# Kernel tuning notes

Hardware: AMD Instinct MI355X
Metric: run time of the kernel (lower is better)

## Reference

```python
import jax, jax.numpy as jnp
import numpy as np

FEAT = 64
K = 16
K4 = K // 4
EPS = 1e-5  # BatchNorm eps (inference mode with running stats)


def _conv1x1(x, w, b):
    # x: (B, Cin, N, K), w: (Cout, Cin), b: (Cout,)
    return jnp.einsum('oc,bcnk->bonk', w, x) + b[None, :, None, None]


def _bn(x, g, be, m, v):
    # inference-mode BatchNorm2d over channel axis 1
    inv = g / jnp.sqrt(v + EPS)
    return (x - m[None, :, None, None]) * inv[None, :, None, None] + be[None, :, None, None]


def setup_inputs() -> dict:
    key = jax.random.key(0)
    ks = jax.random.split(key, 20)
    B, N, M = 4, 8192, 8192
    d = {}
    d['original_pts'] = jax.random.normal(ks[0], (B, 3, M), dtype=jnp.float32)
    d['query_pts'] = jax.random.normal(ks[1], (B, 3, N), dtype=jnp.float32)
    d['local_feat'] = jax.random.normal(ks[2], (B, FEAT, M), dtype=jnp.float32)
    # mlp_0: Conv2D(3, FEAT) with BN + ReLU
    d['w0'] = jax.random.normal(ks[3], (FEAT, 3), dtype=jnp.float32) * 0.2
    d['b0'] = jax.random.normal(ks[4], (FEAT,), dtype=jnp.float32) * 0.01
    d['g0'] = 1.0 + 0.1 * jax.random.normal(ks[5], (FEAT,), dtype=jnp.float32)
    d['be0'] = 0.01 * jax.random.normal(ks[6], (FEAT,), dtype=jnp.float32)
    d['m0'] = 0.01 * jax.random.normal(ks[7], (FEAT,), dtype=jnp.float32)
    d['v0'] = jax.random.uniform(ks[8], (FEAT,), dtype=jnp.float32, minval=0.5, maxval=1.5)
    # mlp_1: Conv2D(FEAT, FEAT) with BN + ReLU
    d['w1'] = jax.random.normal(ks[9], (FEAT, FEAT), dtype=jnp.float32) * 0.1
    d['b1'] = jax.random.normal(ks[10], (FEAT,), dtype=jnp.float32) * 0.01
    d['g1'] = 1.0 + 0.1 * jax.random.normal(ks[11], (FEAT,), dtype=jnp.float32)
    d['be1'] = 0.01 * jax.random.normal(ks[12], (FEAT,), dtype=jnp.float32)
    d['m1'] = 0.01 * jax.random.normal(ks[13], (FEAT,), dtype=jnp.float32)
    d['v1'] = jax.random.uniform(ks[14], (FEAT,), dtype=jnp.float32, minval=0.5, maxval=1.5)
    # mlp_2: Conv2D(2*FEAT, 1), no BN, no ReLU
    d['w2'] = jax.random.normal(ks[15], (1, 2 * FEAT), dtype=jnp.float32) * 0.1
    d['b2'] = jax.random.normal(ks[16], (1,), dtype=jnp.float32) * 0.01
    return d


def reference(original_pts, query_pts, local_feat,
              w0, b0, g0, be0, m0, v0,
              w1, b1, g1, be1, m1, v1,
              w2, b2):
    B, _, N = query_pts.shape
    # --- KNN: squared distances (B, N, M), take K smallest ---
    q2 = jnp.sum(query_pts ** 2, axis=1)          # (B, N)
    o2 = jnp.sum(original_pts ** 2, axis=1)       # (B, M)
    cross = jnp.einsum('bcn,bcm->bnm', query_pts, original_pts)
    d2 = q2[:, :, None] + o2[:, None, :] - 2.0 * cross
    _, knn_idx = jax.lax.top_k(-d2, K)            # (B, N, K)

    # gather neighbor coords: (B, 3, N, K)
    knn_pts = jax.vmap(lambda pts, idx: pts[:, idx])(original_pts, knn_idx)
    # gather local features for first K//4 neighbors: (B, FEAT, N, K4)
    patch_feat = jax.vmap(lambda f, idx: f[:, idx])(local_feat, knn_idx[:, :, :K4])

    relative_pts = knn_pts - query_pts[:, :, :, None]  # (B, 3, N, K)
    feat0 = jax.nn.relu(_bn(_conv1x1(relative_pts, w0, b0), g0, be0, m0, v0))  # (B, F, N, K)
    feat_g = jnp.max(feat0, axis=3, keepdims=True)                              # (B, F, N, 1)
    relative_feat = jax.nn.relu(_bn(_conv1x1(feat0, w1, b1), g1, be1, m1, v1))[:, :, :, :K4]
    feat2 = jnp.concatenate(
        [relative_feat, jnp.broadcast_to(feat_g, (B, FEAT, N, K4))], axis=1)    # (B, 2F, N, K4)
    weight = jax.nn.sigmoid(_conv1x1(feat2, w2, b2))                            # (B, 1, N, K4)
    query_feat = (1.0 - weight) * relative_feat + weight * patch_feat
    return jnp.sum(query_feat, axis=-1)  # (B, FEAT, N)
```

## Files before the change

### kernel.cpp

```cpp
#include <hip/hip_runtime.h>
#include <cstdint>

#define M_PTS 8192
#define N_QRY 8192
#define BATCH 4

typedef unsigned long long ull;

__device__ __forceinline__ float d2_exact(float qx, float qy, float qz, float q2, float4 p) {
#pragma clang fp contract(off)
  float dot = (qx * p.x + qy * p.y) + qz * p.z;
  return (q2 + p.w) - 2.0f * dot;
}

__device__ __forceinline__ unsigned flipf(float d) {
  unsigned u = __float_as_uint(d);
  return u ^ ((unsigned)((int)u >> 31) | 0x80000000u);
}

__device__ __forceinline__ int lane_prefix(unsigned long long m) {
  return __builtin_amdgcn_mbcnt_hi((unsigned)(m >> 32),
         __builtin_amdgcn_mbcnt_lo((unsigned)m, 0));
}

__device__ __forceinline__ void ld_lds16(const float4* g, float4* l) {
  __builtin_amdgcn_global_load_lds((const __attribute__((address_space(1))) void*)g,
                                   (__attribute__((address_space(3))) void*)l, 16, 0, 0);
}

__device__ __forceinline__ float tau16(float mn) {
  float lo = mn, hi = mn;
#pragma unroll
  for (int j = 1; j < 64; j <<= 1) {
    lo = fminf(lo, __shfl_xor(lo, j));
    hi = fmaxf(hi, __shfl_xor(hi, j));
  }
#pragma unroll
  for (int it = 0; it < 10; it++) {
    float mid = 0.5f * (lo + hi);
    int cnt = __popcll(__ballot(mn <= mid));
    if (cnt >= 16) hi = mid; else lo = mid;
  }
  return hi;
}

__device__ __forceinline__ ull bsort64(ull v, int lane) {
#pragma unroll
  for (int k = 2; k <= 64; k <<= 1) {
#pragma unroll
    for (int j = k >> 1; j >= 1; j >>= 1) {
      ull o = __shfl_xor(v, j);
      bool keepmin = (((lane & k) == 0) == ((lane & j) == 0));
      ull lo = v < o ? v : o;
      ull hi = v < o ? o : v;
      v = keepmin ? lo : hi;
    }
  }
  return v;
}

__global__ void prep_kernel(const float* __restrict__ original_pts,
                            const float* __restrict__ query_pts,
                            const float* __restrict__ lf,
                            float4* __restrict__ pp, float4* __restrict__ qp,
                            float* __restrict__ lfT) {
#pragma clang fp contract(off)
  const int bid = blockIdx.x;
  if (bid < 256) {
    const float* src = (bid < 128) ? original_pts : query_pts;
    float4* dst = (bid < 128) ? pp : qp;
    int i = (bid & 127) * 256 + threadIdx.x;
    int b = i >> 13, m = i & (M_PTS - 1);
    const float* s = src + (size_t)b * 3 * M_PTS;
    float x = s[m], y = s[M_PTS + m], z = s[2 * M_PTS + m];
    float ss = (x * x + y * y) + z * z;
    dst[i] = make_float4(x, y, z, ss);
    return;
  }
  __shared__ float tile[64][65];
  int vbid = bid - 256;
  int bb = vbid >> 7;
  int m0 = (vbid & 127) << 6;
  int tm = threadIdx.x & 63;
  int tc = threadIdx.x >> 6;
  const float* src = lf + (size_t)bb * 64 * M_PTS;
#pragma unroll
  for (int i = 0; i < 16; i++) {
    int ch = i * 4 + tc;
    tile[ch][tm] = src[(size_t)ch * M_PTS + m0 + tm];
  }
  __syncthreads();
  float* dst = lfT + ((size_t)bb * M_PTS + m0) * 64;
#pragma unroll
  for (int i = 0; i < 16; i++) {
    int mm = i * 4 + tc;
    dst[(size_t)mm * 64 + tm] = tile[tm][mm];
  }
}

__global__ void __launch_bounds__(512, 8) knn_kernel(const float4* __restrict__ pp,
                                                     const float4* __restrict__ qp,
                                                     int* __restrict__ knn_out,
                                                     int qbase) {
  __shared__ float4 spts[2][512];
  __shared__ ull cbuf[16][96];
  const int tid = threadIdx.x;
  const int lane = tid & 63;
  const int wave = tid >> 6;
  const int qa = qbase + blockIdx.x * 16 + wave * 2;
  const int b = qa >> 13;
  const float4* pb = pp + ((size_t)b << 13);

  const float4 A4 = qp[qa];
  const float4 B4 = qp[qa + 1];
  const float axA = -2.0f * A4.x, ayA = -2.0f * A4.y, azA = -2.0f * A4.z;
  const float axB = -2.0f * B4.x, ayB = -2.0f * B4.y, azB = -2.0f * B4.z;

  int cntA = 0, cntB = 0;
  unsigned* cqA = (unsigned*)cbuf[wave * 2 + 0];
  unsigned* cqB = (unsigned*)cbuf[wave * 2 + 1];

  float mnA = 3.402823466e38f, mnB = 3.402823466e38f;
  float tauA = 0.0f, tauB = 0.0f;

  auto stage = [&](float4* dst, int s) {
    const float4* g = pb + s * 512 + wave * 64 + lane;
    ld_lds16(g, &dst[wave * 64]);
  };

  auto minpass = [&](const float4* sp) {
#pragma unroll
    for (int j = 0; j < 8; j++) {
      float4 p = sp[j * 64 + lane];
      mnA = fminf(mnA, __builtin_fmaf(axA, p.x, __builtin_fmaf(ayA, p.y,
                       __builtin_fmaf(azA, p.z, p.w))));
      mnB = fminf(mnB, __builtin_fmaf(axB, p.x, __builtin_fmaf(ayB, p.y,
                       __builtin_fmaf(azB, p.z, p.w))));
    }
  };

  auto collect = [&](float e, float tau, unsigned* cq, int& cnt, unsigned idx) {
    bool pred = e <= tau;
    unsigned long long mask = __ballot(pred);
    if (mask) {
      int pos = cnt + lane_prefix(mask);
      if (pred && pos < 192) cq[pos] = idx;
      cnt += __popcll(mask);
    }
  };

  auto fused = [&](const float4* sp, unsigned base) {
#pragma unroll
    for (int j = 0; j < 8; j++) {
      float4 p = sp[j * 64 + lane];
      float ea = __builtin_fmaf(axA, p.x, __builtin_fmaf(ayA, p.y,
                 __builtin_fmaf(azA, p.z, p.w)));
      float eb = __builtin_fmaf(axB, p.x, __builtin_fmaf(ayB, p.y,
                 __builtin_fmaf(azB, p.z, p.w)));
      mnA = fminf(mnA, ea);
      mnB = fminf(mnB, eb);
      unsigned idx = base + j * 64 + lane;
      collect(ea, tauA, cqA, cntA, idx);
      collect(eb, tauB, cqB, cntB, idx);
    }
  };

  stage(spts[0], 0);
  __syncthreads();
  stage(spts[1], 1);
  minpass(spts[0]);
  __syncthreads();
  minpass(spts[1]);
  tauA = tau16(mnA) + 0.01f;
  tauB = tau16(mnB) + 0.01f;
  fused(spts[0], 0);
  fused(spts[1], 512);
  __syncthreads();
  stage(spts[0], 2);
  __syncthreads();

  for (int s = 2; s < 16; ++s) {
    if (s < 15) stage(spts[(s + 1) & 1], s + 1);
    fused(spts[s & 1], (unsigned)(s * 512));
    if (s == 3 || s == 7 || s == 11) {
      tauA = fminf(tauA, tau16(mnA) + 0.01f);
      tauB = fminf(tauB, tau16(mnB) + 0.01f);
    }
    __syncthreads();
  }

  auto finalize = [&](ull* cb, int cnt, int gq,
                      float qx, float qy, float qz, float q2) {
    unsigned* cu = (unsigned*)cb;
    int E = cnt < 192 ? cnt : 192;
    unsigned i0 = (lane < E) ? cu[lane] : 0u;
    unsigned i1 = (lane + 64 < E) ? cu[lane + 64] : 0u;
    unsigned i2 = (lane + 128 < E) ? cu[lane + 128] : 0u;
    float4 p0 = pb[i0];
    float4 p1 = pb[i1];
    float4 p2 = pb[i2];
    ull k0 = ~0ull, k1 = ~0ull, k2 = ~0ull;
    if (lane < E)
      k0 = ((ull)flipf(d2_exact(qx, qy, qz, q2, p0)) << 32) | i0;
    if (lane + 64 < E)
      k1 = ((ull)flipf(d2_exact(qx, qy, qz, q2, p1)) << 32) | i1;
    if (lane + 128 < E)
      k2 = ((ull)flipf(d2_exact(qx, qy, qz, q2, p2)) << 32) | i2;
    ull ml = k0 < k1 ? k0 : k1;
    if (k2 < ml) ml = k2;
    ull T = __shfl(bsort64(ml, lane), 15);
    int c2 = 0;
    {
      bool pr = k0 <= T; ull m = __ballot(pr);
      int pos = c2 + lane_prefix(m);
      if (pr) cb[pos] = k0;
      c2 += __popcll(m);
    }
    {
      bool pr = k1 <= T; ull m = __ballot(pr);
      int pos = c2 + lane_prefix(m);
      if (pr) cb[pos] = k1;
      c2 += __popcll(m);
    }
    {
      bool pr = k2 <= T; ull m = __ballot(pr);
      int pos = c2 + lane_prefix(m);
      if (pr) cb[pos] = k2;
      c2 += __popcll(m);
    }
    ull kk = (lane < c2) ? cb[lane] : ~0ull;
    ull fin = bsort64(kk, lane);
    if (lane < 16) knn_out[(size_t)gq * 16 + lane] = (int)(unsigned)fin;
  };

  finalize(cbuf[wave * 2 + 0], cntA, qa,     A4.x, A4.y, A4.z, A4.w);
  finalize(cbuf[wave * 2 + 1], cntB, qa + 1, B4.x, B4.y, B4.z, B4.w);
}

__global__ void __launch_bounds__(512) feat_kernel(
    const float4* __restrict__ pp, const float4* __restrict__ qp,
    const int* __restrict__ knn, const float* __restrict__ lfT,
    const float* __restrict__ w0, const float* __restrict__ b0,
    const float* __restrict__ g0, const float* __restrict__ be0,
    const float* __restrict__ m0, const float* __restrict__ v0,
    const float* __restrict__ w1, const float* __restrict__ b1,
    const float* __restrict__ g1, const float* __restrict__ be1,
    const float* __restrict__ m1, const float* __restrict__ v1,
    const float* __restrict__ w2, const float* __restrict__ b2,
    float* __restrict__ out) {
  __shared__ float w1T[64][65];
  __shared__ float4 relbuf[8][16];
  __shared__ float4 f0v[8][64];
  __shared__ float outbuf[64][33];
  const int tid = threadIdx.x;
  const int lane = tid & 63;
  const int wave = tid >> 6;
  const int gq0 = blockIdx.x * 32;
  const int b = gq0 >> 13;

  {
    const float4* w1f4 = (const float4*)w1;
#pragma unroll
    for (int k = 0; k < 2; k++) {
      int linear4 = tid + k * 512;
      int c = linear4 >> 4;
      int c2 = (linear4 & 15) * 4;
      float4 t = w1f4[linear4];
      w1T[c2 + 0][c] = t.x;
      w1T[c2 + 1][c] = t.y;
      w1T[c2 + 2][c] = t.z;
      w1T[c2 + 3][c] = t.w;
    }
  }

  const float inv0 = g0[lane] / sqrtf(v0[lane] + 1e-5f);
  const float w00 = w0[lane * 3 + 0] * inv0;
  const float w01 = w0[lane * 3 + 1] * inv0;
  const float w02 = w0[lane * 3 + 2] * inv0;
  const float bb0 = (b0[lane] - m0[lane]) * inv0 + be0[lane];
  const float inv1 = g1[lane] / sqrtf(v1[lane] + 1e-5f);
  const float bb1 = (b1[lane] - m1[lane]) * inv1 + be1[lane];

  const float w2a = w2[lane], w2b = w2[64 + lane];
  const float bias2 = b2[0];
  const float4* pb = pp + ((size_t)b << 13);
  const float* lfb = lfT + (((size_t)b << 13)) * 64;

  __syncthreads();

  for (int qi = 0; qi < 4; qi++) {
    const int gq = gq0 + wave * 4 + qi;
    const float4 q4 = qp[gq];
    int nk = knn[(size_t)gq * 16 + (lane & 15)];
    float4 pk = pb[nk];
    int i0 = __shfl(nk, 0), i1 = __shfl(nk, 1), i2 = __shfl(nk, 2), i3 = __shfl(nk, 3);
    float p0 = lfb[(size_t)i0 * 64 + lane];
    float p1 = lfb[(size_t)i1 * 64 + lane];
    float p2 = lfb[(size_t)i2 * 64 + lane];
    float p3 = lfb[(size_t)i3 * 64 + lane];

    if (lane < 16)
      relbuf[wave][lane] = make_float4(pk.x - q4.x, pk.y - q4.y, pk.z - q4.z, 0.0f);

    float g = 0.0f, f0 = 0, f1 = 0, f2 = 0, f3 = 0;
#pragma unroll
    for (int k = 0; k < 16; k++) {
      float4 r = relbuf[wave][k];
      float y = fmaxf(0.0f, w00 * r.x + w01 * r.y + w02 * r.z + bb0);
      g = fmaxf(g, y);
      if (k == 0) f0 = y; else if (k == 1) f1 = y;
      else if (k == 2) f2 = y; else if (k == 3) f3 = y;
    }
    f0v[wave][lane] = make_float4(f0, f1, f2, f3);

    float a0 = 0, a1 = 0, a2 = 0, a3 = 0;
#pragma unroll
    for (int c2 = 0; c2 < 64; c2++) {
      float w = w1T[c2][lane];
      float4 fb = f0v[wave][c2];
      a0 = fmaf(w, fb.x, a0); a1 = fmaf(w, fb.y, a1);
      a2 = fmaf(w, fb.z, a2); a3 = fmaf(w, fb.w, a3);
    }
    float r0 = fmaxf(0.0f, fmaf(a0, inv1, bb1));
    float r1 = fmaxf(0.0f, fmaf(a1, inv1, bb1));
    float r2 = fmaxf(0.0f, fmaf(a2, inv1, bb1));
    float r3 = fmaxf(0.0f, fmaf(a3, inv1, bb1));

    float s0 = w2a * r0, s1 = w2a * r1, s2 = w2a * r2, s3 = w2a * r3, tg = w2b * g;
#pragma unroll
    for (int j = 1; j < 64; j <<= 1) {
      s0 += __shfl_xor(s0, j);
      s1 += __shfl_xor(s1, j);
      s2 += __shfl_xor(s2, j);
      s3 += __shfl_xor(s3, j);
      tg += __shfl_xor(tg, j);
    }
    float wk0 = 1.0f / (1.0f + __expf(-(s0 + tg + bias2)));
    float wk1 = 1.0f / (1.0f + __expf(-(s1 + tg + bias2)));
    float wk2 = 1.0f / (1.0f + __expf(-(s2 + tg + bias2)));
    float wk3 = 1.0f / (1.0f + __expf(-(s3 + tg + bias2)));

    float oc = ((1.0f - wk0) * r0 + wk0 * p0)
             + ((1.0f - wk1) * r1 + wk1 * p1)
             + ((1.0f - wk2) * r2 + wk2 * p2)
             + ((1.0f - wk3) * r3 + wk3 * p3);
    outbuf[lane][wave * 4 + qi] = oc;
  }
  __syncthreads();

  int c = tid >> 3, j = tid & 7;
  float4 o4 = make_float4(outbuf[c][j * 4 + 0], outbuf[c][j * 4 + 1],
                          outbuf[c][j * 4 + 2], outbuf[c][j * 4 + 3]);
  *(float4*)(out + (((size_t)(b * 64 + c)) << 13) + (gq0 & (N_QRY - 1)) + j * 4) = o4;
}

extern "C" void kernel_launch(void* const* d_in, const int* in_sizes, int n_in,
                              void* d_out, int out_size, void* d_ws, size_t ws_size,
                              hipStream_t stream) {
  (void)in_sizes; (void)n_in; (void)out_size; (void)ws_size;
  const float* original_pts = (const float*)d_in[0];
  const float* query_pts   = (const float*)d_in[1];
  const float* local_feat  = (const float*)d_in[2];
  const float* w0 = (const float*)d_in[3];
  const float* b0 = (const float*)d_in[4];
  const float* g0 = (const float*)d_in[5];
  const float* be0 = (const float*)d_in[6];
  const float* m0 = (const float*)d_in[7];
  const float* v0 = (const float*)d_in[8];
  const float* w1 = (const float*)d_in[9];
  const float* b1 = (const float*)d_in[10];
  const float* g1 = (const float*)d_in[11];
  const float* be1 = (const float*)d_in[12];
  const float* m1 = (const float*)d_in[13];
  const float* v1 = (const float*)d_in[14];
  const float* w2 = (const float*)d_in[15];
  const float* b2 = (const float*)d_in[16];
  float* out = (float*)d_out;

  char* ws = (char*)d_ws;
  float4* pp  = (float4*)(ws);
  float4* qp  = (float4*)(ws + 524288);
  float*  lfT = (float*)(ws + 1048576);
  int*    knn = (int*)(ws + 9437184);

  prep_kernel<<<768, 256, 0, stream>>>(original_pts, query_pts, local_feat,
                                       pp, qp, lfT);
  knn_kernel<<<1024, 512, 0, stream>>>(pp, qp, knn, 0);
  knn_kernel<<<1024, 512, 0, stream>>>(pp, qp, knn, 16384);
  feat_kernel<<<1024, 512, 0, stream>>>(pp, qp, knn, lfT,
                                        w0, b0, g0, be0, m0, v0,
                                        w1, b1, g1, be1, m1, v1,
                                        w2, b2, out);
}
```

Before: 255.2 us.

## Fuse KNN search and feature MLP into one kernel with shared-memory neighbor indices

Merges the two KNN launches and the feature kernel into a single kernel. Each block finds neighbors for 16 queries, keeps the indices in shared memory, then reuses an aliased shared buffer for the MLP stage. This removes the global KNN index round trip and two launch boundaries. In exchange the union shared-memory footprint (about 31 KB) may lower occupancy for the KNN phase, the w1 transpose setup is now repeated in twice as many blocks, and the output store uses only half the threads.

```diff
diff --git a/kernel.cpp b/kernel.cpp
--- a/kernel.cpp
+++ b/kernel.cpp
@@ -98,148 +98,9 @@
   }
 }
 
-__global__ void __launch_bounds__(512, 8) knn_kernel(const float4* __restrict__ pp,
-                                                     const float4* __restrict__ qp,
-                                                     int* __restrict__ knn_out,
-                                                     int qbase) {
-  __shared__ float4 spts[2][512];
-  __shared__ ull cbuf[16][96];
-  const int tid = threadIdx.x;
-  const int lane = tid & 63;
-  const int wave = tid >> 6;
-  const int qa = qbase + blockIdx.x * 16 + wave * 2;
-  const int b = qa >> 13;
-  const float4* pb = pp + ((size_t)b << 13);
-
-  const float4 A4 = qp[qa];
-  const float4 B4 = qp[qa + 1];
-  const float axA = -2.0f * A4.x, ayA = -2.0f * A4.y, azA = -2.0f * A4.z;
-  const float axB = -2.0f * B4.x, ayB = -2.0f * B4.y, azB = -2.0f * B4.z;
-
-  int cntA = 0, cntB = 0;
-  unsigned* cqA = (unsigned*)cbuf[wave * 2 + 0];
-  unsigned* cqB = (unsigned*)cbuf[wave * 2 + 1];
-
-  float mnA = 3.402823466e38f, mnB = 3.402823466e38f;
-  float tauA = 0.0f, tauB = 0.0f;
-
-  auto stage = [&](float4* dst, int s) {
-    const float4* g = pb + s * 512 + wave * 64 + lane;
-    ld_lds16(g, &dst[wave * 64]);
-  };
-
-  auto minpass = [&](const float4* sp) {
-#pragma unroll
-    for (int j = 0; j < 8; j++) {
-      float4 p = sp[j * 64 + lane];
-      mnA = fminf(mnA, __builtin_fmaf(axA, p.x, __builtin_fmaf(ayA, p.y,
-                       __builtin_fmaf(azA, p.z, p.w))));
-      mnB = fminf(mnB, __builtin_fmaf(axB, p.x, __builtin_fmaf(ayB, p.y,
-                       __builtin_fmaf(azB, p.z, p.w))));
-    }
-  };
-
-  auto collect = [&](float e, float tau, unsigned* cq, int& cnt, unsigned idx) {
-    bool pred = e <= tau;
-    unsigned long long mask = __ballot(pred);
-    if (mask) {
-      int pos = cnt + lane_prefix(mask);
-      if (pred && pos < 192) cq[pos] = idx;
-      cnt += __popcll(mask);
-    }
-  };
-
-  auto fused = [&](const float4* sp, unsigned base) {
-#pragma unroll
-    for (int j = 0; j < 8; j++) {
-      float4 p = sp[j * 64 + lane];
-      float ea = __builtin_fmaf(axA, p.x, __builtin_fmaf(ayA, p.y,
-                 __builtin_fmaf(azA, p.z, p.w)));
-      float eb = __builtin_fmaf(axB, p.x, __builtin_fmaf(ayB, p.y,
-                 __builtin_fmaf(azB, p.z, p.w)));
-      mnA = fminf(mnA, ea);
-      mnB = fminf(mnB, eb);
-      unsigned idx = base + j * 64 + lane;
-      collect(ea, tauA, cqA, cntA, idx);
-      collect(eb, tauB, cqB, cntB, idx);
-    }
-  };
-
-  stage(spts[0], 0);
-  __syncthreads();
-  stage(spts[1], 1);
-  minpass(spts[0]);
-  __syncthreads();
-  minpass(spts[1]);
-  tauA = tau16(mnA) + 0.01f;
-  tauB = tau16(mnB) + 0.01f;
-  fused(spts[0], 0);
-  fused(spts[1], 512);
-  __syncthreads();
-  stage(spts[0], 2);
-  __syncthreads();
-
-  for (int s = 2; s < 16; ++s) {
-    if (s < 15) stage(spts[(s + 1) & 1], s + 1);
-    fused(spts[s & 1], (unsigned)(s * 512));
-    if (s == 3 || s == 7 || s == 11) {
-      tauA = fminf(tauA, tau16(mnA) + 0.01f);
-      tauB = fminf(tauB, tau16(mnB) + 0.01f);
-    }
-    __syncthreads();
-  }
-
-  auto finalize = [&](ull* cb, int cnt, int gq,
-                      float qx, float qy, float qz, float q2) {
-    unsigned* cu = (unsigned*)cb;
-    int E = cnt < 192 ? cnt : 192;
-    unsigned i0 = (lane < E) ? cu[lane] : 0u;
-    unsigned i1 = (lane + 64 < E) ? cu[lane + 64] : 0u;
-    unsigned i2 = (lane + 128 < E) ? cu[lane + 128] : 0u;
-    float4 p0 = pb[i0];
-    float4 p1 = pb[i1];
-    float4 p2 = pb[i2];
-    ull k0 = ~0ull, k1 = ~0ull, k2 = ~0ull;
-    if (lane < E)
-      k0 = ((ull)flipf(d2_exact(qx, qy, qz, q2, p0)) << 32) | i0;
-    if (lane + 64 < E)
-      k1 = ((ull)flipf(d2_exact(qx, qy, qz, q2, p1)) << 32) | i1;
-    if (lane + 128 < E)
-      k2 = ((ull)flipf(d2_exact(qx, qy, qz, q2, p2)) << 32) | i2;
-    ull ml = k0 < k1 ? k0 : k1;
-    if (k2 < ml) ml = k2;
-    ull T = __shfl(bsort64(ml, lane), 15);
-    int c2 = 0;
-    {
-      bool pr = k0 <= T; ull m = __ballot(pr);
-      int pos = c2 + lane_prefix(m);
-      if (pr) cb[pos] = k0;
-      c2 += __popcll(m);
-    }
-    {
-      bool pr = k1 <= T; ull m = __ballot(pr);
-      int pos = c2 + lane_prefix(m);
-      if (pr) cb[pos] = k1;
-      c2 += __popcll(m);
-    }
-    {
-      bool pr = k2 <= T; ull m = __ballot(pr);
-      int pos = c2 + lane_prefix(m);
-      if (pr) cb[pos] = k2;
-      c2 += __popcll(m);
-    }
-    ull kk = (lane < c2) ? cb[lane] : ~0ull;
-    ull fin = bsort64(kk, lane);
-    if (lane < 16) knn_out[(size_t)gq * 16 + lane] = (int)(unsigned)fin;
-  };
-
-  finalize(cbuf[wave * 2 + 0], cntA, qa,     A4.x, A4.y, A4.z, A4.w);
-  finalize(cbuf[wave * 2 + 1], cntB, qa + 1, B4.x, B4.y, B4.z, B4.w);
-}
-
-__global__ void __launch_bounds__(512) feat_kernel(
+__global__ void __launch_bounds__(512) fused_kernel(
     const float4* __restrict__ pp, const float4* __restrict__ qp,
-    const int* __restrict__ knn, const float* __restrict__ lfT,
+    const float* __restrict__ lfT,
     const float* __restrict__ w0, const float* __restrict__ b0,
     const float* __restrict__ g0, const float* __restrict__ be0,
     const float* __restrict__ m0, const float* __restrict__ v0,
@@ -248,15 +109,155 @@
     const float* __restrict__ m1, const float* __restrict__ v1,
     const float* __restrict__ w2, const float* __restrict__ b2,
     float* __restrict__ out) {
-  __shared__ float w1T[64][65];
-  __shared__ float4 relbuf[8][16];
-  __shared__ float4 f0v[8][64];
-  __shared__ float outbuf[64][33];
+  __shared__ __align__(16) char smem[31232];
+  __shared__ int sknn[16][16];
   const int tid = threadIdx.x;
   const int lane = tid & 63;
   const int wave = tid >> 6;
-  const int gq0 = blockIdx.x * 32;
-  const int b = gq0 >> 13;
+  const int gq0 = blockIdx.x * 16;
+  const int qa = gq0 + wave * 2;
+  const int b = qa >> 13;
+  const float4* pb = pp + ((size_t)b << 13);
+
+  {
+    ull (*cbuf)[96] = (ull(*)[96])(smem + 16384);
+
+    const float4 A4 = qp[qa];
+    const float4 B4 = qp[qa + 1];
+    const float axA = -2.0f * A4.x, ayA = -2.0f * A4.y, azA = -2.0f * A4.z;
+    const float axB = -2.0f * B4.x, ayB = -2.0f * B4.y, azB = -2.0f * B4.z;
+
+    int cntA = 0, cntB = 0;
+    unsigned* cqA = (unsigned*)cbuf[wave * 2 + 0];
+    unsigned* cqB = (unsigned*)cbuf[wave * 2 + 1];
+
+    float mnA = 3.402823466e38f, mnB = 3.402823466e38f;
+    float tauA = 0.0f, tauB = 0.0f;
+
+    auto bufp = [&](int d) -> float4* {
+      return (float4*)(smem + ((size_t)d << 13));
+    };
+
+    auto stage = [&](int d, int s) {
+      const float4* g = pb + s * 512 + wave * 64 + lane;
+      ld_lds16(g, bufp(d) + wave * 64);
+    };
+
+    auto minpass = [&](const float4* sp) {
+#pragma unroll
+      for (int j = 0; j < 8; j++) {
+        float4 p = sp[j * 64 + lane];
+        mnA = fminf(mnA, __builtin_fmaf(axA, p.x, __builtin_fmaf(ayA, p.y,
+                         __builtin_fmaf(azA, p.z, p.w))));
+        mnB = fminf(mnB, __builtin_fmaf(axB, p.x, __builtin_fmaf(ayB, p.y,
+                         __builtin_fmaf(azB, p.z, p.w))));
+      }
+    };
+
+    auto collect = [&](float e, float tau, unsigned* cq, int& cnt, unsigned idx) {
+      bool pred = e <= tau;
+      unsigned long long mask = __ballot(pred);
+      if (mask) {
+        int pos = cnt + lane_prefix(mask);
+        if (pred && pos < 192) cq[pos] = idx;
+        cnt += __popcll(mask);
+      }
+    };
+
+    auto fused = [&](const float4* sp, unsigned base) {
+#pragma unroll
+      for (int j = 0; j < 8; j++) {
+        float4 p = sp[j * 64 + lane];
+        float ea = __builtin_fmaf(axA, p.x, __builtin_fmaf(ayA, p.y,
+                   __builtin_fmaf(azA, p.z, p.w)));
+        float eb = __builtin_fmaf(axB, p.x, __builtin_fmaf(ayB, p.y,
+                   __builtin_fmaf(azB, p.z, p.w)));
+        mnA = fminf(mnA, ea);
+        mnB = fminf(mnB, eb);
+        unsigned idx = base + j * 64 + lane;
+        collect(ea, tauA, cqA, cntA, idx);
+        collect(eb, tauB, cqB, cntB, idx);
+      }
+    };
+
+    stage(0, 0);
+    __syncthreads();
+    stage(1, 1);
+    minpass(bufp(0));
+    __syncthreads();
+    minpass(bufp(1));
+    tauA = tau16(mnA) + 0.01f;
+    tauB = tau16(mnB) + 0.01f;
+    fused(bufp(0), 0);
+    fused(bufp(1), 512);
+    __syncthreads();
+    stage(0, 2);
+    __syncthreads();
+
+    for (int s = 2; s < 16; ++s) {
+      if (s < 15) stage((s + 1) & 1, s + 1);
+      fused(bufp(s & 1), (unsigned)(s * 512));
+      if (s == 3 || s == 7 || s == 11) {
+        tauA = fminf(tauA, tau16(mnA) + 0.01f);
+        tauB = fminf(tauB, tau16(mnB) + 0.01f);
+      }
+      __syncthreads();
+    }
+
+    auto finalize = [&](ull* cb, int cnt, int* srow,
+                        float qx, float qy, float qz, float q2) {
+      unsigned* cu = (unsigned*)cb;
+      int E = cnt < 192 ? cnt : 192;
+      unsigned i0 = (lane < E) ? cu[lane] : 0u;
+      unsigned i1 = (lane + 64 < E) ? cu[lane + 64] : 0u;
+      unsigned i2 = (lane + 128 < E) ? cu[lane + 128] : 0u;
+      float4 p0 = pb[i0];
+      float4 p1 = pb[i1];
+      float4 p2 = pb[i2];
+      ull k0 = ~0ull, k1 = ~0ull, k2 = ~0ull;
+      if (lane < E)
+        k0 = ((ull)flipf(d2_exact(qx, qy, qz, q2, p0)) << 32) | i0;
+      if (lane + 64 < E)
+        k1 = ((ull)flipf(d2_exact(qx, qy, qz, q2, p1)) << 32) | i1;
+      if (lane + 128 < E)
+        k2 = ((ull)flipf(d2_exact(qx, qy, qz, q2, p2)) << 32) | i2;
+      ull ml = k0 < k1 ? k0 : k1;
+      if (k2 < ml) ml = k2;
+      ull T = __shfl(bsort64(ml, lane), 15);
+      int c2 = 0;
+      {
+        bool pr = k0 <= T; ull m = __ballot(pr);
+        int pos = c2 + lane_prefix(m);
+        if (pr) cb[pos] = k0;
+        c2 += __popcll(m);
+      }
+      {
+        bool pr = k1 <= T; ull m = __ballot(pr);
+        int pos = c2 + lane_prefix(m);
+        if (pr) cb[pos] = k1;
+        c2 += __popcll(m);
+      }
+      {
+        bool pr = k2 <= T; ull m = __ballot(pr);
+        int pos = c2 + lane_prefix(m);
+        if (pr) cb[pos] = k2;
+        c2 += __popcll(m);
+      }
+      ull kk = (lane < c2) ? cb[lane] : ~0ull;
+      ull fin = bsort64(kk, lane);
+      if (lane < 16) srow[lane] = (int)(unsigned)fin;
+    };
+
+    finalize(cbuf[wave * 2 + 0], cntA, sknn[wave * 2 + 0], A4.x, A4.y, A4.z, A4.w);
+    finalize(cbuf[wave * 2 + 1], cntB, sknn[wave * 2 + 1], B4.x, B4.y, B4.z, B4.w);
+  }
+
+  __syncthreads();
+
+  float (*w1T)[65]    = (float(*)[65])smem;
+  float4 (*relbuf)[16] = (float4(*)[16])(smem + 16640);
+  float4 (*f0v)[64]   = (float4(*)[64])(smem + 18688);
+  float (*outbuf)[17] = (float(*)[17])(smem + 26880);
 
   {
     const float4* w1f4 = (const float4*)w1;
@@ -283,15 +284,14 @@
 
   const float w2a = w2[lane], w2b = w2[64 + lane];
   const float bias2 = b2[0];
-  const float4* pb = pp + ((size_t)b << 13);
   const float* lfb = lfT + (((size_t)b << 13)) * 64;
 
   __syncthreads();
 
-  for (int qi = 0; qi < 4; qi++) {
-    const int gq = gq0 + wave * 4 + qi;
+  for (int qi = 0; qi < 2; qi++) {
+    const int gq = qa + qi;
     const float4 q4 = qp[gq];
-    int nk = knn[(size_t)gq * 16 + (lane & 15)];
+    int nk = sknn[wave * 2 + qi][lane & 15];
     float4 pk = pb[nk];
     int i0 = __shfl(nk, 0), i1 = __shfl(nk, 1), i2 = __shfl(nk, 2), i3 = __shfl(nk, 3);
     float p0 = lfb[(size_t)i0 * 64 + lane];
@@ -344,14 +344,16 @@
              + ((1.0f - wk1) * r1 + wk1 * p1)
              + ((1.0f - wk2) * r2 + wk2 * p2)
              + ((1.0f - wk3) * r3 + wk3 * p3);
-    outbuf[lane][wave * 4 + qi] = oc;
+    outbuf[lane][wave * 2 + qi] = oc;
   }
   __syncthreads();
 
-  int c = tid >> 3, j = tid & 7;
-  float4 o4 = make_float4(outbuf[c][j * 4 + 0], outbuf[c][j * 4 + 1],
-                          outbuf[c][j * 4 + 2], outbuf[c][j * 4 + 3]);
-  *(float4*)(out + (((size_t)(b * 64 + c)) << 13) + (gq0 & (N_QRY - 1)) + j * 4) = o4;
+  if (tid < 256) {
+    int c = tid >> 2, j = tid & 3;
+    float4 o4 = make_float4(outbuf[c][j * 4 + 0], outbuf[c][j * 4 + 1],
+                            outbuf[c][j * 4 + 2], outbuf[c][j * 4 + 3]);
+    *(float4*)(out + (((size_t)(b * 64 + c)) << 13) + (gq0 & (N_QRY - 1)) + j * 4) = o4;
+  }
 }
 
 extern "C" void kernel_launch(void* const* d_in, const int* in_sizes, int n_in,
@@ -381,14 +383,11 @@
   float4* pp  = (float4*)(ws);
   float4* qp  = (float4*)(ws + 524288);
   float*  lfT = (float*)(ws + 1048576);
-  int*    knn = (int*)(ws + 9437184);
 
   prep_kernel<<<768, 256, 0, stream>>>(original_pts, query_pts, local_feat,
                                        pp, qp, lfT);
-  knn_kernel<<<1024, 512, 0, stream>>>(pp, qp, knn, 0);
-  knn_kernel<<<1024, 512, 0, stream>>>(pp, qp, knn, 16384);
-  feat_kernel<<<1024, 512, 0, stream>>>(pp, qp, knn, lfT,
-                                        w0, b0, g0, be0, m0, v0,
-                                        w1, b1, g1, be1, m1, v1,
-                                        w2, b2, out);
-}
+  fused_kernel<<<2048, 512, 0, stream>>>(pp, qp, lfT,
+                                         w0, b0, g0, be0, m0, v0,
+                                         w1, b1, g1, be1, m1, v1,
+                                         w2, b2, out);
+}
```

New measurement: 246.1 us, median of 2. 3.6% less time.
